# Kernel optimization log

Measured on AMD Instinct MI355X. Metric: run time of the kernel, lower is better.

## Reference

```python
import jax, jax.numpy as jnp
import numpy as np

SIZE = 11
SIGMA = 1.5
C1 = 0.01 ** 2
C2 = 0.03 ** 2


def gaussian_kernel(size, sigma):
    x, y = np.mgrid[-size:size + 1, -size:size + 1]
    k = np.exp(-0.5 * (x * x + y * y) / (sigma * sigma))
    return (k / k.sum()).astype(np.float32)


def _dwconv(x, w, pad):
    # depthwise conv, NCHW input, OIHW kernel (C,1,kh,kw)
    return jax.lax.conv_general_dilated(
        x, w, window_strides=(1, 1), padding=[(pad, pad), (pad, pad)],
        dimension_numbers=('NCHW', 'OIHW', 'NCHW'),
        feature_group_count=x.shape[1])


def setup_inputs() -> dict:
    key = jax.random.key(0)
    k1, k2 = jax.random.split(key)
    B, C, H, W = 16, 3, 512, 512
    inp = jax.random.uniform(k1, (B, C, H, W), dtype=jnp.float32)
    tgt = jax.random.uniform(k2, (B, C, H, W), dtype=jnp.float32)
    kern = gaussian_kernel(SIZE, SIGMA)  # (23,23)
    weight = jnp.asarray(np.tile(kern, (C, 1, 1, 1)))  # (C,1,23,23)
    return {"input": inp, "target": tgt, "weight": weight}


def reference(input, target, weight):
    pad = SIZE
    mean1 = _dwconv(input, weight, pad)
    mean2 = _dwconv(target, weight, pad)
    mean1_sq = mean1 * mean1
    mean2_sq = mean2 * mean2
    mean_12 = mean1 * mean2
    sigma1_sq = _dwconv(input * input, weight, pad) - mean1_sq
    sigma2_sq = _dwconv(target * target, weight, pad) - mean2_sq
    sigma_12 = _dwconv(input * target, weight, pad) - mean_12
    ssim = (2 * mean_12 + C1) * (2 * sigma_12 + C2) / (
        (mean1_sq + mean2_sq + C1) * (sigma1_sq + sigma2_sq + C2))
    return 1.0 - ssim.mean()
```

## Files before the change

### kernel.cpp

```cpp
#include <hip/hip_runtime.h>
#include <hip/hip_bf16.h>

typedef float f32x4 __attribute__((ext_vector_type(4)));
typedef short bf16x8 __attribute__((ext_vector_type(8)));

#define HH 512
#define WW 512
#define NPLANES 48
#define KSIZE 23
#define NBLK (16 * 16 * NPLANES)
#define C1V 1.0e-4f
#define C2V 9.0e-4f

#define SB_O   0
#define SA_O   3960
#define G_O    7920
#define HB_O   9968
#define HB_CH  2048
#define SPITCH 72
#define LDS_TOT 20208

#define SWZ(rho, k) ((k) ^ (((rho) & 7) << 3))

__device__ __forceinline__ unsigned cvtpk(float a, float b) {
    union { __hip_bfloat162 h; unsigned u; } cv;
    cv.h = __float22bfloat162_rn(make_float2(a, b));
    return cv.u;
}

__device__ __forceinline__ unsigned bfmul2(unsigned a, unsigned b) {
    float al = __uint_as_float(a << 16), ah = __uint_as_float(a & 0xffff0000u);
    float bl = __uint_as_float(b << 16), bh = __uint_as_float(b & 0xffff0000u);
    return cvtpk(al * bl, ah * bh);
}

__device__ __forceinline__ uint4 bfmul4(uint4 a, uint4 b) {
    uint4 r;
    r.x = bfmul2(a.x, b.x); r.y = bfmul2(a.y, b.y);
    r.z = bfmul2(a.z, b.z); r.w = bfmul2(a.w, b.w);
    return r;
}

__device__ __forceinline__ f32x4 mfma16(uint4 a, uint4 b, f32x4 c) {
    union { uint4 u; bf16x8 h; } ua, ub;
    ua.u = a; ub.u = b;
    return __builtin_amdgcn_mfma_f32_16x16x32_bf16(ua.h, ub.h, c, 0, 0, 0);
}

__global__ __launch_bounds__(256, 4) void ssim_main_kernel(
    const float* __restrict__ in, const float* __restrict__ tg,
    const float* __restrict__ w, float* __restrict__ partial)
{
    __shared__ __align__(16) unsigned short lds[LDS_TOT];
    __shared__ float swsum[4];

    const int tid = threadIdx.x;
    const int wave = tid >> 6, lane = tid & 63;
    const int m = lane & 15, q = lane >> 4;

    const int blk = blockIdx.x;
    const int plane = blk >> 8;
    const int t2 = blk & 255;
    const int x0 = (t2 & 15) * 32 - 12;
    const int y0 = (t2 >> 4) * 32 - 12;
    const float* __restrict__ inp = in + (size_t)plane * (HH * WW);
    const float* __restrict__ tgp = tg + (size_t)plane * (HH * WW);

    const bool interior = (x0 >= 0) && (y0 >= 0) && (x0 + 64 <= WW) && (y0 + 55 <= HH);

    float4 La[2][2], Lb[2][2];
    if (interior) {
        #pragma unroll
        for (int it = 0; it < 2; ++it) {
            int t = tid + it * 256;
            if (t < 440) {
                int r = t >> 3, c8 = (t & 7) << 3;
                const float4* pa = (const float4*)(inp + (y0 + r) * WW + x0 + c8);
                const float4* pb = (const float4*)(tgp + (y0 + r) * WW + x0 + c8);
                La[it][0] = pa[0]; La[it][1] = pa[1];
                Lb[it][0] = pb[0]; Lb[it][1] = pb[1];
            }
        }
    }

    float gv = 0.f;
    if (lane < KSIZE) {
        #pragma unroll
        for (int k = 0; k < KSIZE; ++k) gv += w[lane * KSIZE + k];
    }
    {
        unsigned* gw = (unsigned*)lds + (G_O >> 1);
        const int kd = lane & 31;
        const int rh = (lane >> 5) << 2;
        #pragma unroll
        for (int i = 0; i < 4; ++i) {
            int r = wave * 8 + rh + i;
            int d0 = 2 * kd - 1 - r;
            float g0 = __shfl(gv, d0 & 63, 64);
            float g1 = __shfl(gv, (d0 + 1) & 63, 64);
            g0 = ((unsigned)d0 < (unsigned)KSIZE) ? g0 : 0.f;
            g1 = ((unsigned)(d0 + 1) < (unsigned)KSIZE) ? g1 : 0.f;
            gw[r * 32 + (kd ^ ((r & 7) << 2))] = cvtpk(g0, g1);
        }
    }

    if (interior) {
        #pragma unroll
        for (int it = 0; it < 2; ++it) {
            int t = tid + it * 256;
            if (t < 440) {
                int r = t >> 3, c8 = (t & 7) << 3;
                uint4 va, vb;
                va.x = cvtpk(La[it][0].x, La[it][0].y); va.y = cvtpk(La[it][0].z, La[it][0].w);
                va.z = cvtpk(La[it][1].x, La[it][1].y); va.w = cvtpk(La[it][1].z, La[it][1].w);
                vb.x = cvtpk(Lb[it][0].x, Lb[it][0].y); vb.y = cvtpk(Lb[it][0].z, Lb[it][0].w);
                vb.z = cvtpk(Lb[it][1].x, Lb[it][1].y); vb.w = cvtpk(Lb[it][1].z, Lb[it][1].w);
                *(uint4*)&lds[SA_O + r * SPITCH + c8] = va;
                *(uint4*)&lds[SB_O + r * SPITCH + c8] = vb;
            }
        }
    } else {
        unsigned* ldsw = (unsigned*)lds;
        for (int t = tid; t < 55 * 32; t += 256) {
            int r = t >> 5, cd = t & 31;
            int gy = y0 + r, gx = x0 + cd * 2;
            float a0 = 0.f, a1 = 0.f, b0 = 0.f, b1 = 0.f;
            if (gy >= 0 && gy < HH) {
                const float* ri = inp + gy * WW;
                const float* rt = tgp + gy * WW;
                if ((unsigned)gx < (unsigned)WW)       { a0 = ri[gx];     b0 = rt[gx]; }
                if ((unsigned)(gx + 1) < (unsigned)WW) { a1 = ri[gx + 1]; b1 = rt[gx + 1]; }
            }
            ldsw[(SA_O >> 1) + r * 36 + cd] = cvtpk(a0, a1);
            ldsw[(SB_O >> 1) + r * 36 + cd] = cvtpk(b0, b1);
        }
    }
    __syncthreads();

    f32x4 acc5[5][2];
    const f32x4 zz = {0.f, 0.f, 0.f, 0.f};
    #pragma unroll
    for (int ch = 0; ch < 5; ++ch) { acc5[ch][0] = zz; acc5[ch][1] = zz; }

    #pragma unroll
    for (int ks = 0; ks < 2; ++ks) {
        const int off = (wave * 16 + m) * SPITCH + ks * 32 + q * 8;
        uint4 ua = *(const uint4*)&lds[SA_O + off];
        uint4 ub = *(const uint4*)&lds[SB_O + off];
        uint4 uaa = bfmul4(ua, ua);
        uint4 ubb = bfmul4(ub, ub);
        uint4 uab = bfmul4(ua, ub);
        #pragma unroll
        for (int nc = 0; nc < 2; ++nc) {
            const int gr = nc * 16 + m;
            uint4 gf = *(const uint4*)&lds[G_O + gr * 64 + SWZ(gr, ks * 32 + q * 8)];
            acc5[0][nc] = mfma16(ua,  gf, acc5[0][nc]);
            acc5[1][nc] = mfma16(ub,  gf, acc5[1][nc]);
            acc5[2][nc] = mfma16(uaa, gf, acc5[2][nc]);
            acc5[3][nc] = mfma16(ubb, gf, acc5[3][nc]);
            acc5[4][nc] = mfma16(uab, gf, acc5[4][nc]);
        }
    }
    #pragma unroll
    for (int ch = 0; ch < 5; ++ch)
        #pragma unroll
        for (int nc = 0; nc < 2; ++nc) {
            f32x4 a = acc5[ch][nc];
            uint2 pk;
            pk.x = cvtpk(a[0], a[1]);
            pk.y = cvtpk(a[2], a[3]);
            const int col = nc * 16 + m;
            const int rb = wave * 16 + q * 4;
            *(uint2*)&lds[HB_O + ch * HB_CH + col * 64 + SWZ(col, rb)] = pk;
        }
    __syncthreads();

    const int mrow = wave >> 1, nc2 = wave & 1;
    f32x4 av[5];
    #pragma unroll
    for (int ch = 0; ch < 5; ++ch) av[ch] = zz;

    #pragma unroll
    for (int ks = 0; ks < 2; ++ks) {
        const int ar = mrow * 16 + m;
        uint4 ga = *(const uint4*)&lds[G_O + ar * 64 + SWZ(ar, ks * 32 + q * 8)];
        #pragma unroll
        for (int ch = 0; ch < 5; ++ch) {
            const int col = nc2 * 16 + m;
            uint4 ub = *(const uint4*)&lds[HB_O + ch * HB_CH + col * 64 + SWZ(col, ks * 32 + q * 8)];
            av[ch] = mfma16(ga, ub, av[ch]);
        }
    }

    float lsum = 0.f;
    #pragma unroll
    for (int i = 0; i < 4; ++i) {
        float vx = av[0][i], vt = av[1][i];
        float vxx = av[2][i], vtt = av[3][i], vxt = av[4][i];
        float m1s = vx * vx, m2s = vt * vt, m12 = vx * vt;
        float s1 = vxx - m1s, s2 = vtt - m2s, s12 = vxt - m12;
        float num = (2.f * m12 + C1V) * (2.f * s12 + C2V);
        float den = (m1s + m2s + C1V) * (s1 + s2 + C2V);
        lsum += num * __builtin_amdgcn_rcpf(den);
    }
    #pragma unroll
    for (int off = 32; off > 0; off >>= 1)
        lsum += __shfl_down(lsum, off, 64);
    if (lane == 0) swsum[wave] = lsum;
    __syncthreads();
    if (tid == 0)
        partial[blk] = swsum[0] + swsum[1] + swsum[2] + swsum[3];
}

__global__ __launch_bounds__(256) void ssim_final_kernel(
    const float* __restrict__ partial, float* __restrict__ out)
{
    __shared__ float swsum[4];
    const int tid = threadIdx.x;
    float s = 0.f;
    const float4* p4 = (const float4*)partial;
    for (int i = tid; i < NBLK / 4; i += 256) {
        float4 v = p4[i];
        s += (v.x + v.y) + (v.z + v.w);
    }
    #pragma unroll
    for (int off = 32; off > 0; off >>= 1)
        s += __shfl_down(s, off, 64);
    if ((tid & 63) == 0) swsum[tid >> 6] = s;
    __syncthreads();
    if (tid == 0)
        out[0] = 1.0f - (swsum[0] + swsum[1] + swsum[2] + swsum[3])
                        * (1.0f / ((float)NPLANES * HH * WW));
}

extern "C" void kernel_launch(void* const* d_in, const int* in_sizes, int n_in,
                              void* d_out, int out_size, void* d_ws, size_t ws_size,
                              hipStream_t stream) {
    const float* inp = (const float*)d_in[0];
    const float* tgt = (const float*)d_in[1];
    const float* wgt = (const float*)d_in[2];
    float* out = (float*)d_out;
    float* partial = (float*)d_ws;

    ssim_main_kernel<<<NBLK, 256, 0, stream>>>(inp, tgt, wgt, partial);
    ssim_final_kernel<<<1, 256, 0, stream>>>(partial, out);
}
```

Baseline: 179.5 us.

## Merge squared-sum channels, load inputs directly to registers, precompute Gaussian band matrix

The SSIM terms only need the sum of filtered x² and filtered y², so the two squared channels are merged into one. That cuts the MFMA passes and the intermediate LDS buffers from five to four. Input tiles are now loaded from global memory straight into MFMA operand registers, which removes the staging LDS buffers and one barrier. The band matrix built from the Gaussian weights is now computed once by a separate prep kernel and read from global memory. The goal is to lower LDS use so occupancy can be raised to 6 blocks per CU. In exchange there is an extra kernel launch, global reads of the matrix in every block, and some tile rows are loaded twice because overlapping waves no longer share them through LDS.

```diff
diff --git a/kernel.cpp b/kernel.cpp
--- a/kernel.cpp
+++ b/kernel.cpp
@@ -12,13 +12,7 @@
 #define C1V 1.0e-4f
 #define C2V 9.0e-4f
 
-#define SB_O   0
-#define SA_O   3960
-#define G_O    7920
-#define HB_O   9968
-#define HB_CH  2048
-#define SPITCH 72
-#define LDS_TOT 20208
+#define HB_CH 2048
 
 #define SWZ(rho, k) ((k) ^ (((rho) & 7) << 3))
 
@@ -28,17 +22,12 @@
     return cv.u;
 }
 
-__device__ __forceinline__ unsigned bfmul2(unsigned a, unsigned b) {
+__device__ __forceinline__ void prod2(unsigned a, unsigned b,
+                                      unsigned& pab, unsigned& pss) {
     float al = __uint_as_float(a << 16), ah = __uint_as_float(a & 0xffff0000u);
     float bl = __uint_as_float(b << 16), bh = __uint_as_float(b & 0xffff0000u);
-    return cvtpk(al * bl, ah * bh);
-}
-
-__device__ __forceinline__ uint4 bfmul4(uint4 a, uint4 b) {
-    uint4 r;
-    r.x = bfmul2(a.x, b.x); r.y = bfmul2(a.y, b.y);
-    r.z = bfmul2(a.z, b.z); r.w = bfmul2(a.w, b.w);
-    return r;
+    pab = cvtpk(al * bl, ah * bh);
+    pss = cvtpk(al * al + bl * bl, ah * ah + bh * bh);
 }
 
 __device__ __forceinline__ f32x4 mfma16(uint4 a, uint4 b, f32x4 c) {
@@ -47,11 +36,31 @@
     return __builtin_amdgcn_mfma_f32_16x16x32_bf16(ua.h, ub.h, c, 0, 0, 0);
 }
 
-__global__ __launch_bounds__(256, 4) void ssim_main_kernel(
+__global__ __launch_bounds__(64) void ssim_prep_kernel(
+    const float* __restrict__ w, unsigned* __restrict__ Gg)
+{
+    const int lane = threadIdx.x;
+    float gv = 0.f;
+    if (lane < KSIZE) {
+        #pragma unroll
+        for (int k = 0; k < KSIZE; ++k) gv += w[lane * KSIZE + k];
+    }
+    for (int idx = lane; idx < 32 * 32; idx += 64) {
+        int r = idx >> 5, kd = idx & 31;
+        int d0 = 2 * kd - 1 - r;
+        float g0 = __shfl(gv, d0 & 63, 64);
+        float g1 = __shfl(gv, (d0 + 1) & 63, 64);
+        g0 = ((unsigned)d0 < (unsigned)KSIZE) ? g0 : 0.f;
+        g1 = ((unsigned)(d0 + 1) < (unsigned)KSIZE) ? g1 : 0.f;
+        Gg[idx] = cvtpk(g0, g1);
+    }
+}
+
+__global__ __launch_bounds__(256, 6) void ssim_main_kernel(
     const float* __restrict__ in, const float* __restrict__ tg,
-    const float* __restrict__ w, float* __restrict__ partial)
+    const unsigned* __restrict__ Gg, float* __restrict__ partial)
 {
-    __shared__ __align__(16) unsigned short lds[LDS_TOT];
+    __shared__ __align__(16) unsigned short hb[4 * HB_CH];
     __shared__ float swsum[4];
 
     const int tid = threadIdx.x;
@@ -66,128 +75,82 @@
     const float* __restrict__ inp = in + (size_t)plane * (HH * WW);
     const float* __restrict__ tgp = tg + (size_t)plane * (HH * WW);
 
-    const bool interior = (x0 >= 0) && (y0 >= 0) && (x0 + 64 <= WW) && (y0 + 55 <= HH);
-
-    float4 La[2][2], Lb[2][2];
-    if (interior) {
-        #pragma unroll
-        for (int it = 0; it < 2; ++it) {
-            int t = tid + it * 256;
-            if (t < 440) {
-                int r = t >> 3, c8 = (t & 7) << 3;
-                const float4* pa = (const float4*)(inp + (y0 + r) * WW + x0 + c8);
-                const float4* pb = (const float4*)(tgp + (y0 + r) * WW + x0 + c8);
-                La[it][0] = pa[0]; La[it][1] = pa[1];
-                Lb[it][0] = pb[0]; Lb[it][1] = pb[1];
+    const int row = y0 + wave * 16 + m;
+    const bool rowOK = ((unsigned)row < (unsigned)HH);
+    const bool xin = (x0 >= 0) && (x0 + 64 <= WW);
+
+    f32x4 acc[4][2];
+    const f32x4 zz = {0.f, 0.f, 0.f, 0.f};
+    #pragma unroll
+    for (int ch = 0; ch < 4; ++ch) { acc[ch][0] = zz; acc[ch][1] = zz; }
+
+    #pragma unroll
+    for (int ks = 0; ks < 2; ++ks) {
+        const int cb = x0 + ks * 32 + q * 8;
+        float4 z4; z4.x = z4.y = z4.z = z4.w = 0.f;
+        float4 fa0 = z4, fa1 = z4, fb0 = z4, fb1 = z4;
+        if (xin) {
+            if (rowOK) {
+                const float* ri = inp + row * WW + cb;
+                const float* rt = tgp + row * WW + cb;
+                fa0 = ((const float4*)ri)[0]; fa1 = ((const float4*)ri)[1];
+                fb0 = ((const float4*)rt)[0]; fb1 = ((const float4*)rt)[1];
             }
-        }
-    }
-
-    float gv = 0.f;
-    if (lane < KSIZE) {
-        #pragma unroll
-        for (int k = 0; k < KSIZE; ++k) gv += w[lane * KSIZE + k];
-    }
-    {
-        unsigned* gw = (unsigned*)lds + (G_O >> 1);
-        const int kd = lane & 31;
-        const int rh = (lane >> 5) << 2;
-        #pragma unroll
-        for (int i = 0; i < 4; ++i) {
-            int r = wave * 8 + rh + i;
-            int d0 = 2 * kd - 1 - r;
-            float g0 = __shfl(gv, d0 & 63, 64);
-            float g1 = __shfl(gv, (d0 + 1) & 63, 64);
-            g0 = ((unsigned)d0 < (unsigned)KSIZE) ? g0 : 0.f;
-            g1 = ((unsigned)(d0 + 1) < (unsigned)KSIZE) ? g1 : 0.f;
-            gw[r * 32 + (kd ^ ((r & 7) << 2))] = cvtpk(g0, g1);
-        }
-    }
-
-    if (interior) {
-        #pragma unroll
-        for (int it = 0; it < 2; ++it) {
-            int t = tid + it * 256;
-            if (t < 440) {
-                int r = t >> 3, c8 = (t & 7) << 3;
-                uint4 va, vb;
-                va.x = cvtpk(La[it][0].x, La[it][0].y); va.y = cvtpk(La[it][0].z, La[it][0].w);
-                va.z = cvtpk(La[it][1].x, La[it][1].y); va.w = cvtpk(La[it][1].z, La[it][1].w);
-                vb.x = cvtpk(Lb[it][0].x, Lb[it][0].y); vb.y = cvtpk(Lb[it][0].z, Lb[it][0].w);
-                vb.z = cvtpk(Lb[it][1].x, Lb[it][1].y); vb.w = cvtpk(Lb[it][1].z, Lb[it][1].w);
-                *(uint4*)&lds[SA_O + r * SPITCH + c8] = va;
-                *(uint4*)&lds[SB_O + r * SPITCH + c8] = vb;
+        } else if (rowOK) {
+            const float* ri = inp + row * WW;
+            const float* rt = tgp + row * WW;
+            if (cb >= 0 && cb + 4 <= WW) {
+                fa0 = *(const float4*)(ri + cb);     fb0 = *(const float4*)(rt + cb);
             }
-        }
-    } else {
-        unsigned* ldsw = (unsigned*)lds;
-        for (int t = tid; t < 55 * 32; t += 256) {
-            int r = t >> 5, cd = t & 31;
-            int gy = y0 + r, gx = x0 + cd * 2;
-            float a0 = 0.f, a1 = 0.f, b0 = 0.f, b1 = 0.f;
-            if (gy >= 0 && gy < HH) {
-                const float* ri = inp + gy * WW;
-                const float* rt = tgp + gy * WW;
-                if ((unsigned)gx < (unsigned)WW)       { a0 = ri[gx];     b0 = rt[gx]; }
-                if ((unsigned)(gx + 1) < (unsigned)WW) { a1 = ri[gx + 1]; b1 = rt[gx + 1]; }
+            if (cb + 4 >= 0 && cb + 8 <= WW) {
+                fa1 = *(const float4*)(ri + cb + 4); fb1 = *(const float4*)(rt + cb + 4);
             }
-            ldsw[(SA_O >> 1) + r * 36 + cd] = cvtpk(a0, a1);
-            ldsw[(SB_O >> 1) + r * 36 + cd] = cvtpk(b0, b1);
-        }
-    }
-    __syncthreads();
-
-    f32x4 acc5[5][2];
-    const f32x4 zz = {0.f, 0.f, 0.f, 0.f};
-    #pragma unroll
-    for (int ch = 0; ch < 5; ++ch) { acc5[ch][0] = zz; acc5[ch][1] = zz; }
-
-    #pragma unroll
-    for (int ks = 0; ks < 2; ++ks) {
-        const int off = (wave * 16 + m) * SPITCH + ks * 32 + q * 8;
-        uint4 ua = *(const uint4*)&lds[SA_O + off];
-        uint4 ub = *(const uint4*)&lds[SB_O + off];
-        uint4 uaa = bfmul4(ua, ua);
-        uint4 ubb = bfmul4(ub, ub);
-        uint4 uab = bfmul4(ua, ub);
+        }
+        uint4 ua, ub, uab, uss;
+        ua.x = cvtpk(fa0.x, fa0.y); ua.y = cvtpk(fa0.z, fa0.w);
+        ua.z = cvtpk(fa1.x, fa1.y); ua.w = cvtpk(fa1.z, fa1.w);
+        ub.x = cvtpk(fb0.x, fb0.y); ub.y = cvtpk(fb0.z, fb0.w);
+        ub.z = cvtpk(fb1.x, fb1.y); ub.w = cvtpk(fb1.z, fb1.w);
+        prod2(ua.x, ub.x, uab.x, uss.x);
+        prod2(ua.y, ub.y, uab.y, uss.y);
+        prod2(ua.z, ub.z, uab.z, uss.z);
+        prod2(ua.w, ub.w, uab.w, uss.w);
         #pragma unroll
         for (int nc = 0; nc < 2; ++nc) {
-            const int gr = nc * 16 + m;
-            uint4 gf = *(const uint4*)&lds[G_O + gr * 64 + SWZ(gr, ks * 32 + q * 8)];
-            acc5[0][nc] = mfma16(ua,  gf, acc5[0][nc]);
-            acc5[1][nc] = mfma16(ub,  gf, acc5[1][nc]);
-            acc5[2][nc] = mfma16(uaa, gf, acc5[2][nc]);
-            acc5[3][nc] = mfma16(ubb, gf, acc5[3][nc]);
-            acc5[4][nc] = mfma16(uab, gf, acc5[4][nc]);
-        }
-    }
-    #pragma unroll
-    for (int ch = 0; ch < 5; ++ch)
+            uint4 gf = *(const uint4*)(Gg + (nc * 16 + m) * 32 + ks * 16 + q * 4);
+            acc[0][nc] = mfma16(ua,  gf, acc[0][nc]);
+            acc[1][nc] = mfma16(ub,  gf, acc[1][nc]);
+            acc[2][nc] = mfma16(uss, gf, acc[2][nc]);
+            acc[3][nc] = mfma16(uab, gf, acc[3][nc]);
+        }
+    }
+
+    #pragma unroll
+    for (int ch = 0; ch < 4; ++ch)
         #pragma unroll
         for (int nc = 0; nc < 2; ++nc) {
-            f32x4 a = acc5[ch][nc];
+            f32x4 a = acc[ch][nc];
             uint2 pk;
             pk.x = cvtpk(a[0], a[1]);
             pk.y = cvtpk(a[2], a[3]);
             const int col = nc * 16 + m;
             const int rb = wave * 16 + q * 4;
-            *(uint2*)&lds[HB_O + ch * HB_CH + col * 64 + SWZ(col, rb)] = pk;
+            *(uint2*)&hb[ch * HB_CH + col * 64 + SWZ(col, rb)] = pk;
         }
     __syncthreads();
 
     const int mrow = wave >> 1, nc2 = wave & 1;
-    f32x4 av[5];
-    #pragma unroll
-    for (int ch = 0; ch < 5; ++ch) av[ch] = zz;
+    f32x4 av[4];
+    #pragma unroll
+    for (int ch = 0; ch < 4; ++ch) av[ch] = zz;
 
     #pragma unroll
     for (int ks = 0; ks < 2; ++ks) {
-        const int ar = mrow * 16 + m;
-        uint4 ga = *(const uint4*)&lds[G_O + ar * 64 + SWZ(ar, ks * 32 + q * 8)];
-        #pragma unroll
-        for (int ch = 0; ch < 5; ++ch) {
+        uint4 ga = *(const uint4*)(Gg + (mrow * 16 + m) * 32 + ks * 16 + q * 4);
+        #pragma unroll
+        for (int ch = 0; ch < 4; ++ch) {
             const int col = nc2 * 16 + m;
-            uint4 ub = *(const uint4*)&lds[HB_O + ch * HB_CH + col * 64 + SWZ(col, ks * 32 + q * 8)];
+            uint4 ub = *(const uint4*)&hb[ch * HB_CH + col * 64 + SWZ(col, ks * 32 + q * 8)];
             av[ch] = mfma16(ga, ub, av[ch]);
         }
     }
@@ -196,11 +159,12 @@
     #pragma unroll
     for (int i = 0; i < 4; ++i) {
         float vx = av[0][i], vt = av[1][i];
-        float vxx = av[2][i], vtt = av[3][i], vxt = av[4][i];
+        float vss = av[2][i], vxt = av[3][i];
         float m1s = vx * vx, m2s = vt * vt, m12 = vx * vt;
-        float s1 = vxx - m1s, s2 = vtt - m2s, s12 = vxt - m12;
+        float sss = vss - m1s - m2s;
+        float s12 = vxt - m12;
         float num = (2.f * m12 + C1V) * (2.f * s12 + C2V);
-        float den = (m1s + m2s + C1V) * (s1 + s2 + C2V);
+        float den = (m1s + m2s + C1V) * (sss + C2V);
         lsum += num * __builtin_amdgcn_rcpf(den);
     }
     #pragma unroll
@@ -241,7 +205,9 @@
     const float* wgt = (const float*)d_in[2];
     float* out = (float*)d_out;
     float* partial = (float*)d_ws;
-
-    ssim_main_kernel<<<NBLK, 256, 0, stream>>>(inp, tgt, wgt, partial);
+    unsigned* Gg = (unsigned*)((char*)d_ws + NBLK * sizeof(float));
+
+    ssim_prep_kernel<<<1, 64, 0, stream>>>(wgt, Gg);
+    ssim_main_kernel<<<NBLK, 256, 0, stream>>>(inp, tgt, Gg, partial);
     ssim_final_kernel<<<1, 256, 0, stream>>>(partial, out);
 }
```

Result: slower. 195.3 us (+8.8%).

## Merge squared channels, reuse input LDS for intermediates, precompute Gaussian band matrix

Applied to the files above, without the earlier changes.

Because only sigma1_sq + sigma2_sq appears in the SSIM formula, the x² and t² channels are fused into one x²+t² channel. That cuts the MFMA convolution passes from 5 to 4 and shrinks the horizontal-pass buffer. The intermediate buffer now overlays the input tiles, guarded by an extra barrier, which roughly halves LDS per block so launch bounds can go from 4 to 6 blocks per CU. The banded Gaussian matrix is built once by a small prep kernel into workspace and copied into LDS, rather than rebuilt by every block. The costs are an extra kernel launch, an extra __syncthreads, and a small bf16 precision change from summing squares before rounding.

```diff
diff --git a/kernel.cpp b/kernel.cpp
--- a/kernel.cpp
+++ b/kernel.cpp
@@ -14,11 +14,12 @@
 
 #define SB_O   0
 #define SA_O   3960
-#define G_O    7920
-#define HB_O   9968
+#define OV_O   7920
+#define G_O    8568
+#define HB_O   0
 #define HB_CH  2048
 #define SPITCH 72
-#define LDS_TOT 20208
+#define LDS_TOT 10616
 
 #define SWZ(rho, k) ((k) ^ (((rho) & 7) << 3))
 
@@ -28,17 +29,12 @@
     return cv.u;
 }
 
-__device__ __forceinline__ unsigned bfmul2(unsigned a, unsigned b) {
+__device__ __forceinline__ void prod2(unsigned a, unsigned b,
+                                      unsigned& pab, unsigned& pss) {
     float al = __uint_as_float(a << 16), ah = __uint_as_float(a & 0xffff0000u);
     float bl = __uint_as_float(b << 16), bh = __uint_as_float(b & 0xffff0000u);
-    return cvtpk(al * bl, ah * bh);
-}
-
-__device__ __forceinline__ uint4 bfmul4(uint4 a, uint4 b) {
-    uint4 r;
-    r.x = bfmul2(a.x, b.x); r.y = bfmul2(a.y, b.y);
-    r.z = bfmul2(a.z, b.z); r.w = bfmul2(a.w, b.w);
-    return r;
+    pab = cvtpk(al * bl, ah * bh);
+    pss = cvtpk(al * al + bl * bl, ah * ah + bh * bh);
 }
 
 __device__ __forceinline__ f32x4 mfma16(uint4 a, uint4 b, f32x4 c) {
@@ -47,9 +43,29 @@
     return __builtin_amdgcn_mfma_f32_16x16x32_bf16(ua.h, ub.h, c, 0, 0, 0);
 }
 
-__global__ __launch_bounds__(256, 4) void ssim_main_kernel(
+__global__ __launch_bounds__(64) void ssim_prep_kernel(
+    const float* __restrict__ w, unsigned* __restrict__ Gg)
+{
+    const int lane = threadIdx.x;
+    float gv = 0.f;
+    if (lane < KSIZE) {
+        #pragma unroll
+        for (int k = 0; k < KSIZE; ++k) gv += w[lane * KSIZE + k];
+    }
+    for (int idx = lane; idx < 32 * 32; idx += 64) {
+        int r = idx >> 5, kd = idx & 31;
+        int d0 = 2 * kd - 1 - r;
+        float g0 = __shfl(gv, d0 & 63, 64);
+        float g1 = __shfl(gv, (d0 + 1) & 63, 64);
+        g0 = ((unsigned)d0 < (unsigned)KSIZE) ? g0 : 0.f;
+        g1 = ((unsigned)(d0 + 1) < (unsigned)KSIZE) ? g1 : 0.f;
+        Gg[idx] = cvtpk(g0, g1);
+    }
+}
+
+__global__ __launch_bounds__(256, 6) void ssim_main_kernel(
     const float* __restrict__ in, const float* __restrict__ tg,
-    const float* __restrict__ w, float* __restrict__ partial)
+    const unsigned* __restrict__ Gg, float* __restrict__ partial)
 {
     __shared__ __align__(16) unsigned short lds[LDS_TOT];
     __shared__ float swsum[4];
@@ -83,25 +99,15 @@
         }
     }
 
-    float gv = 0.f;
-    if (lane < KSIZE) {
-        #pragma unroll
-        for (int k = 0; k < KSIZE; ++k) gv += w[lane * KSIZE + k];
-    }
     {
-        unsigned* gw = (unsigned*)lds + (G_O >> 1);
-        const int kd = lane & 31;
-        const int rh = (lane >> 5) << 2;
-        #pragma unroll
-        for (int i = 0; i < 4; ++i) {
-            int r = wave * 8 + rh + i;
-            int d0 = 2 * kd - 1 - r;
-            float g0 = __shfl(gv, d0 & 63, 64);
-            float g1 = __shfl(gv, (d0 + 1) & 63, 64);
-            g0 = ((unsigned)d0 < (unsigned)KSIZE) ? g0 : 0.f;
-            g1 = ((unsigned)(d0 + 1) < (unsigned)KSIZE) ? g1 : 0.f;
-            gw[r * 32 + (kd ^ ((r & 7) << 2))] = cvtpk(g0, g1);
-        }
+        int r = tid >> 3;
+        int dc = (tid & 7) << 2;
+        uint4 g4 = *(const uint4*)(Gg + r * 32 + dc);
+        *(uint4*)&lds[G_O + r * 64 + (((dc << 1)) ^ ((r & 7) << 3))] = g4;
+    }
+    if (tid < 81) {
+        uint4 z; z.x = z.y = z.z = z.w = 0u;
+        *(uint4*)&lds[OV_O + tid * 8] = z;
     }
 
     if (interior) {
@@ -137,35 +143,38 @@
     }
     __syncthreads();
 
-    f32x4 acc5[5][2];
+    f32x4 acc[4][2];
     const f32x4 zz = {0.f, 0.f, 0.f, 0.f};
     #pragma unroll
-    for (int ch = 0; ch < 5; ++ch) { acc5[ch][0] = zz; acc5[ch][1] = zz; }
+    for (int ch = 0; ch < 4; ++ch) { acc[ch][0] = zz; acc[ch][1] = zz; }
 
     #pragma unroll
     for (int ks = 0; ks < 2; ++ks) {
         const int off = (wave * 16 + m) * SPITCH + ks * 32 + q * 8;
         uint4 ua = *(const uint4*)&lds[SA_O + off];
         uint4 ub = *(const uint4*)&lds[SB_O + off];
-        uint4 uaa = bfmul4(ua, ua);
-        uint4 ubb = bfmul4(ub, ub);
-        uint4 uab = bfmul4(ua, ub);
+        uint4 uab, uss;
+        prod2(ua.x, ub.x, uab.x, uss.x);
+        prod2(ua.y, ub.y, uab.y, uss.y);
+        prod2(ua.z, ub.z, uab.z, uss.z);
+        prod2(ua.w, ub.w, uab.w, uss.w);
         #pragma unroll
         for (int nc = 0; nc < 2; ++nc) {
             const int gr = nc * 16 + m;
             uint4 gf = *(const uint4*)&lds[G_O + gr * 64 + SWZ(gr, ks * 32 + q * 8)];
-            acc5[0][nc] = mfma16(ua,  gf, acc5[0][nc]);
-            acc5[1][nc] = mfma16(ub,  gf, acc5[1][nc]);
-            acc5[2][nc] = mfma16(uaa, gf, acc5[2][nc]);
-            acc5[3][nc] = mfma16(ubb, gf, acc5[3][nc]);
-            acc5[4][nc] = mfma16(uab, gf, acc5[4][nc]);
-        }
-    }
-    #pragma unroll
-    for (int ch = 0; ch < 5; ++ch)
+            acc[0][nc] = mfma16(ua,  gf, acc[0][nc]);
+            acc[1][nc] = mfma16(ub,  gf, acc[1][nc]);
+            acc[2][nc] = mfma16(uss, gf, acc[2][nc]);
+            acc[3][nc] = mfma16(uab, gf, acc[3][nc]);
+        }
+    }
+    __syncthreads();
+
+    #pragma unroll
+    for (int ch = 0; ch < 4; ++ch)
         #pragma unroll
         for (int nc = 0; nc < 2; ++nc) {
-            f32x4 a = acc5[ch][nc];
+            f32x4 a = acc[ch][nc];
             uint2 pk;
             pk.x = cvtpk(a[0], a[1]);
             pk.y = cvtpk(a[2], a[3]);
@@ -176,16 +185,16 @@
     __syncthreads();
 
     const int mrow = wave >> 1, nc2 = wave & 1;
-    f32x4 av[5];
-    #pragma unroll
-    for (int ch = 0; ch < 5; ++ch) av[ch] = zz;
+    f32x4 av[4];
+    #pragma unroll
+    for (int ch = 0; ch < 4; ++ch) av[ch] = zz;
 
     #pragma unroll
     for (int ks = 0; ks < 2; ++ks) {
         const int ar = mrow * 16 + m;
         uint4 ga = *(const uint4*)&lds[G_O + ar * 64 + SWZ(ar, ks * 32 + q * 8)];
         #pragma unroll
-        for (int ch = 0; ch < 5; ++ch) {
+        for (int ch = 0; ch < 4; ++ch) {
             const int col = nc2 * 16 + m;
             uint4 ub = *(const uint4*)&lds[HB_O + ch * HB_CH + col * 64 + SWZ(col, ks * 32 + q * 8)];
             av[ch] = mfma16(ga, ub, av[ch]);
@@ -196,11 +205,12 @@
     #pragma unroll
     for (int i = 0; i < 4; ++i) {
         float vx = av[0][i], vt = av[1][i];
-        float vxx = av[2][i], vtt = av[3][i], vxt = av[4][i];
+        float vss = av[2][i], vxt = av[3][i];
         float m1s = vx * vx, m2s = vt * vt, m12 = vx * vt;
-        float s1 = vxx - m1s, s2 = vtt - m2s, s12 = vxt - m12;
+        float sss = vss - m1s - m2s;
+        float s12 = vxt - m12;
         float num = (2.f * m12 + C1V) * (2.f * s12 + C2V);
-        float den = (m1s + m2s + C1V) * (s1 + s2 + C2V);
+        float den = (m1s + m2s + C1V) * (sss + C2V);
         lsum += num * __builtin_amdgcn_rcpf(den);
     }
     #pragma unroll
@@ -241,7 +251,9 @@
     const float* wgt = (const float*)d_in[2];
     float* out = (float*)d_out;
     float* partial = (float*)d_ws;
-
-    ssim_main_kernel<<<NBLK, 256, 0, stream>>>(inp, tgt, wgt, partial);
+    unsigned* Gg = (unsigned*)((char*)d_ws + NBLK * sizeof(float));
+
+    ssim_prep_kernel<<<1, 64, 0, stream>>>(wgt, Gg);
+    ssim_main_kernel<<<NBLK, 256, 0, stream>>>(inp, tgt, Gg, partial);
     ssim_final_kernel<<<1, 256, 0, stream>>>(partial, out);
 }
```

After: 157.5 us. 12.3% less time.
